# Optimization experiments

Hardware: AMD Instinct MI355X
Metric: run time of the kernel (lower is better)

Reference implementation:

```python
import jax, jax.numpy as jnp
import numpy as np

B, NQ, NKV = 2, 2048, 2048
DIM, CTX_DIM = 1024, 1024
HEADS, DIM_HEAD = 16, 64
INNER = HEADS * DIM_HEAD  # 1024
SCALE = DIM_HEAD ** -0.5


def setup_inputs() -> dict:
    key = jax.random.key(0)
    ks = jax.random.split(key, 6)
    x = jax.random.normal(ks[0], (B, NQ, DIM), dtype=jnp.float32)
    context = jax.random.normal(ks[1], (B, NKV, CTX_DIM), dtype=jnp.float32)
    # nn.Linear weights stored as [out, in] in torch; we keep [in, out] for x @ W.
    Wq = jax.random.normal(ks[2], (DIM, INNER), dtype=jnp.float32) / np.sqrt(DIM)
    Wkv = jax.random.normal(ks[3], (CTX_DIM, 2 * INNER), dtype=jnp.float32) / np.sqrt(CTX_DIM)
    Wout = jax.random.normal(ks[4], (INNER, DIM), dtype=jnp.float32) / np.sqrt(INNER)
    bout = jax.random.normal(ks[5], (DIM,), dtype=jnp.float32) * 0.01
    return {"x": x, "context": context, "Wq": Wq, "Wkv": Wkv, "Wout": Wout, "bout": bout}


def reference(x, context, Wq, Wkv, Wout, bout):
    q = x @ Wq                      # [B, Nq, inner]
    kv = context @ Wkv              # [B, Nkv, 2*inner]
    k, v = jnp.split(kv, 2, axis=-1)

    def split_heads(t):             # [B, N, inner] -> [B, H, N, dh]
        return t.reshape(t.shape[0], t.shape[1], HEADS, DIM_HEAD).transpose(0, 2, 1, 3)

    q, k, v = split_heads(q), split_heads(k), split_heads(v)
    dots = jnp.einsum('bhqd,bhkd->bhqk', q, k) * SCALE  # [B, H, Nq, Nkv]
    attn = jax.nn.softmax(dots, axis=-1)
    out = jnp.einsum('bhqk,bhkd->bhqd', attn, v)        # [B, H, Nq, dh]
    out = out.transpose(0, 2, 1, 3).reshape(out.shape[0], out.shape[2], INNER)
    return out @ Wout + bout        # [B, Nq, dim]
```

## Files before the change

### kernel.cpp

```cpp
#include <hip/hip_runtime.h>
#include <hip/hip_bf16.h>
#include <stdint.h>

#define NQ 2048
#define NKV 2048
#define DIM 1024
#define INNER 1024
#define HEADS 16
#define DH 64
#define BATCH 2

typedef float f32x4 __attribute__((ext_vector_type(4)));
typedef __bf16 bf16x8 __attribute__((ext_vector_type(8)));
typedef unsigned int u32x4 __attribute__((ext_vector_type(4)));

__device__ inline ushort f2b(float f) {
    uint32_t u = __builtin_bit_cast(uint32_t, f);
    u += 0x7fff + ((u >> 16) & 1);
    return (ushort)(u >> 16);
}

__device__ inline uint pkbf16(float lo, float hi) {
    __hip_bfloat162 h = __float22bfloat162_rn(make_float2(lo, hi));
    uint r;
    __builtin_memcpy(&r, &h, 4);
    return r;
}

__device__ __forceinline__ void gload16(const void* g, void* lds) {
    __builtin_amdgcn_global_load_lds(
        (const __attribute__((address_space(1))) unsigned int*)g,
        (__attribute__((address_space(3))) unsigned int*)lds, 16, 0, 0);
}

__global__ void cvt_f32_bf16(const float* __restrict__ in, ushort* __restrict__ out, int n4) {
    int i = blockIdx.x * blockDim.x + threadIdx.x;
    int stride = gridDim.x * blockDim.x;
    for (; i < n4; i += stride) {
        float4 v = ((const float4*)in)[i];
        ushort4 o;
        o.x = f2b(v.x); o.y = f2b(v.y); o.z = f2b(v.z); o.w = f2b(v.w);
        ((ushort4*)out)[i] = o;
    }
}

__global__ void transp_cvt(const float* __restrict__ in, ushort* __restrict__ out, int R, int C) {
    __shared__ ushort tile[32][33];
    int c0 = blockIdx.x * 32, r0 = blockIdx.y * 32;
    int tx = threadIdx.x, ty = threadIdx.y;
#pragma unroll
    for (int i = 0; i < 4; i++)
        tile[ty + i * 8][tx] = f2b(in[(size_t)(r0 + ty + i * 8) * C + c0 + tx]);
    __syncthreads();
#pragma unroll
    for (int i = 0; i < 4; i++)
        out[(size_t)(c0 + ty + i * 8) * R + r0 + tx] = tile[tx][ty + i * 8];
}

__global__ __launch_bounds__(256) void vtransp(const ushort* __restrict__ vb, ushort* __restrict__ vtb) {
    __shared__ ushort tile[64][72];
    int kt = blockIdx.x, h = blockIdx.y, b = blockIdx.z;
    int t = threadIdx.x;
    const ushort* src = vb + ((size_t)b * NKV + kt * 64) * INNER + h * DH;
#pragma unroll
    for (int p = 0; p < 2; p++) {
        int kv = p * 32 + (t >> 3), c0 = (t & 7) * 8;
        u32x4 v = *(const u32x4*)&src[(size_t)kv * INNER + c0];
        *(u32x4*)&tile[kv][c0] = v;
    }
    __syncthreads();
    ushort* dst = vtb + (((size_t)b * HEADS + h) * DH) * NKV + kt * 64;
#pragma unroll
    for (int p = 0; p < 2; p++) {
        int d = p * 32 + (t >> 3), k0 = (t & 7) * 8;
        ushort tmp[8];
#pragma unroll
        for (int j = 0; j < 8; j++) tmp[j] = tile[k0 + j][d];
        *(u32x4*)&dst[(size_t)d * NKV + k0] = *(u32x4*)tmp;
    }
}

template <int MODE, int BN>
__global__ __launch_bounds__(256) void gemm_bt(const ushort* __restrict__ A, const ushort* __restrict__ Bt,
                                               void* __restrict__ C0, void* __restrict__ C1,
                                               const float* __restrict__ bias, float oscale,
                                               int M, int N, int K) {
    constexpr int NI = BN / 32;
    __shared__ ushort As[2][4096];
    __shared__ ushort Bs[2][BN * 32];
    int m0 = blockIdx.y * 128, n0 = blockIdx.x * BN;
    int t = threadIdx.x, l = t & 63, w = t >> 6;
    int wr = w >> 1, wc = w & 1;
    int lg = l >> 4, lc = l & 15;
    f32x4 acc[4][NI] = {};

    auto stage = [&](int buf, int k0) {
#pragma unroll
        for (int i = 0; i < 2; i++) {
            int s = w + i * 4;
            gload16(A + (size_t)(m0 + (s & 1) * 64 + l) * K + k0 + (s >> 1) * 8, &As[buf][s * 512]);
        }
        if (BN == 128) {
#pragma unroll
            for (int i = 0; i < 2; i++) {
                int s = w + i * 4;
                gload16(Bt + (size_t)(n0 + (s & 1) * 64 + l) * K + k0 + (s >> 1) * 8, &Bs[buf][s * 512]);
            }
        } else {
            gload16(Bt + (size_t)(n0 + l) * K + k0 + w * 8, &Bs[buf][w * 512]);
        }
    };

    stage(0, 0);
    for (int k0 = 0, tt = 0; k0 < K; k0 += 32, ++tt) {
        __syncthreads();
        int cur = tt & 1;
        if (k0 + 32 < K) stage(cur ^ 1, k0 + 32);
        bf16x8 af[4], bf[NI];
#pragma unroll
        for (int mi = 0; mi < 4; mi++)
            af[mi] = *(const bf16x8*)&As[cur][(lg * 128 + wr * 64 + mi * 16 + lc) * 8];
#pragma unroll
        for (int ni = 0; ni < NI; ni++)
            bf[ni] = *(const bf16x8*)&Bs[cur][(lg * BN + wc * (BN / 2) + ni * 16 + lc) * 8];
        __builtin_amdgcn_s_setprio(1);
#pragma unroll
        for (int mi = 0; mi < 4; mi++)
#pragma unroll
            for (int ni = 0; ni < NI; ni++)
                acc[mi][ni] = __builtin_amdgcn_mfma_f32_16x16x32_bf16(af[mi], bf[ni], acc[mi][ni], 0, 0, 0);
        __builtin_amdgcn_s_setprio(0);
    }
#pragma unroll
    for (int mi = 0; mi < 4; mi++)
#pragma unroll
        for (int ni = 0; ni < NI; ni++)
#pragma unroll
            for (int r = 0; r < 4; r++) {
                int m = m0 + wr * 64 + mi * 16 + lg * 4 + r;
                int n = n0 + wc * (BN / 2) + ni * 16 + lc;
                float v = acc[mi][ni][r];
                if (MODE == 0) {
                    ((ushort*)C0)[(size_t)m * N + n] = f2b(v * oscale);
                } else if (MODE == 1) {
                    if (n < 1024) ((ushort*)C0)[(size_t)m * 1024 + n] = f2b(v);
                    else          ((ushort*)C1)[(size_t)m * 1024 + (n - 1024)] = f2b(v);
                } else {
                    ((float*)C0)[(size_t)m * N + n] = v + bias[n];
                }
            }
}

__global__ __launch_bounds__(256, 3) void attn3(const ushort* __restrict__ qb, const ushort* __restrict__ kb,
                                                const ushort* __restrict__ vtb, ushort* __restrict__ ob) {
    __shared__ ushort Qs[8 * 128 * 8];
    __shared__ ushort Ks[2][4096];
    __shared__ ushort Vs[2][4096];
    uint* Psw = (uint*)Qs;
    int flat = blockIdx.x;
    int swz = (flat & 7) * 64 + (flat >> 3);
    int qt = swz & 15, h = (swz >> 4) & 15, b = swz >> 8;
    int t = threadIdx.x, l = t & 63, w = t >> 6;
    int lg = l >> 4, lc = l & 15;
    int xsw = (lc << 1) & 0x1C;
    const ushort* Qg = qb + (size_t)b * NQ * INNER + h * DH;
    const ushort* Kg = kb + (size_t)b * NKV * INNER + h * DH;
    const ushort* Vg = vtb + (((size_t)b * HEADS + h) * DH) * NKV;
    int q0 = qt * 128;

#pragma unroll
    for (int i = 0; i < 4; i++) {
        int s = w * 4 + i;
        gload16(Qg + (size_t)(q0 + (s & 1) * 64 + l) * INNER + (s >> 1) * 8, &Qs[s * 512]);
    }
    auto stageKV = [&](int buf, int kv0) {
#pragma unroll
        for (int i = 0; i < 2; i++) {
            int s = w + i * 4;
            gload16(Kg + (size_t)(kv0 + l) * INNER + s * 8, &Ks[buf][s * 512]);
            gload16(Vg + (size_t)l * NKV + kv0 + s * 8, &Vs[buf][s * 512]);
        }
    };
    stageKV(0, 0);
    __syncthreads();

    bf16x8 qf[2][2];
#pragma unroll
    for (int mi = 0; mi < 2; mi++)
#pragma unroll
        for (int kc = 0; kc < 2; kc++)
            qf[mi][kc] = *(const bf16x8*)&Qs[((kc * 4 + lg) * 128 + w * 32 + mi * 16 + lc) * 8];
    __syncthreads();

    uint* Ps = Psw + w * 1024;
    f32x4 o[2][4] = {};
    float m_[2] = {-1e30f, -1e30f}, s_[2] = {0.f, 0.f};

    for (int tt = 0; tt < NKV / 64; ++tt) {
        int cur = tt & 1;
        if (tt + 1 < NKV / 64) stageKV(cur ^ 1, (tt + 1) * 64);
        f32x4 st[2][4] = {};
        __builtin_amdgcn_s_setprio(1);
#pragma unroll
        for (int kc = 0; kc < 2; kc++)
#pragma unroll
            for (int nb = 0; nb < 4; nb++) {
                bf16x8 kf = *(const bf16x8*)&Ks[cur][((kc * 4 + lg) * 64 + nb * 16 + lc) * 8];
                st[0][nb] = __builtin_amdgcn_mfma_f32_16x16x32_bf16(kf, qf[0][kc], st[0][nb], 0, 0, 0);
                st[1][nb] = __builtin_amdgcn_mfma_f32_16x16x32_bf16(kf, qf[1][kc], st[1][nb], 0, 0, 0);
            }
        __builtin_amdgcn_s_setprio(0);
#pragma unroll
        for (int mi = 0; mi < 2; mi++) {
            float mx = st[mi][0][0];
#pragma unroll
            for (int nb = 0; nb < 4; nb++)
#pragma unroll
                for (int r = 0; r < 4; r++) mx = fmaxf(mx, st[mi][nb][r]);
            mx = fmaxf(mx, __shfl_xor(mx, 16));
            mx = fmaxf(mx, __shfl_xor(mx, 32));
            float mn = fmaxf(m_[mi], mx);
            float fac = __builtin_amdgcn_exp2f(m_[mi] - mn);
            m_[mi] = mn;
            s_[mi] *= fac;
#pragma unroll
            for (int nb = 0; nb < 4; nb++) o[mi][nb] *= fac;
            float rs = 0.f;
#pragma unroll
            for (int nb = 0; nb < 4; nb++) {
                float p0 = __builtin_amdgcn_exp2f(st[mi][nb][0] - mn);
                float p1 = __builtin_amdgcn_exp2f(st[mi][nb][1] - mn);
                float p2 = __builtin_amdgcn_exp2f(st[mi][nb][2] - mn);
                float p3 = __builtin_amdgcn_exp2f(st[mi][nb][3] - mn);
                rs += (p0 + p1) + (p2 + p3);
                uint2 pw;
                pw.x = pkbf16(p0, p1);
                pw.y = pkbf16(p2, p3);
                *(uint2*)&Ps[(mi * 16 + lc) * 32 + ((nb * 8 + lg * 2) ^ xsw)] = pw;
            }
            rs += __shfl_xor(rs, 16);
            rs += __shfl_xor(rs, 32);
            s_[mi] += rs;
        }
        asm volatile("" ::: "memory");
        bf16x8 pf[2][2], vf[4][2];
#pragma unroll
        for (int mi = 0; mi < 2; mi++)
#pragma unroll
            for (int kc = 0; kc < 2; kc++)
                pf[mi][kc] = *(const bf16x8*)&Ps[(mi * 16 + lc) * 32 + ((kc * 16 + lg * 4) ^ xsw)];
#pragma unroll
        for (int nb = 0; nb < 4; nb++)
#pragma unroll
            for (int kc = 0; kc < 2; kc++)
                vf[nb][kc] = *(const bf16x8*)&Vs[cur][((kc * 4 + lg) * 64 + nb * 16 + lc) * 8];
        __builtin_amdgcn_s_setprio(1);
#pragma unroll
        for (int nb = 0; nb < 4; nb++)
#pragma unroll
            for (int kc = 0; kc < 2; kc++) {
                o[0][nb] = __builtin_amdgcn_mfma_f32_16x16x32_bf16(vf[nb][kc], pf[0][kc], o[0][nb], 0, 0, 0);
                o[1][nb] = __builtin_amdgcn_mfma_f32_16x16x32_bf16(vf[nb][kc], pf[1][kc], o[1][nb], 0, 0, 0);
            }
        __builtin_amdgcn_s_setprio(0);
        __syncthreads();
    }
    ushort* Og = ob + (size_t)b * NQ * INNER + h * DH;
#pragma unroll
    for (int mi = 0; mi < 2; mi++) {
        float inv = 1.f / s_[mi];
        int q = q0 + w * 32 + mi * 16 + lc;
#pragma unroll
        for (int nb = 0; nb < 4; nb++) {
            uint2 pw;
            pw.x = pkbf16(o[mi][nb][0] * inv, o[mi][nb][1] * inv);
            pw.y = pkbf16(o[mi][nb][2] * inv, o[mi][nb][3] * inv);
            *(uint2*)&Og[(size_t)q * INNER + nb * 16 + lg * 4] = pw;
        }
    }
}

extern "C" void kernel_launch(void* const* d_in, const int* in_sizes, int n_in,
                              void* d_out, int out_size, void* d_ws, size_t ws_size,
                              hipStream_t stream) {
    const float* x    = (const float*)d_in[0];
    const float* ctx  = (const float*)d_in[1];
    const float* Wq   = (const float*)d_in[2];
    const float* Wkv  = (const float*)d_in[3];
    const float* Wout = (const float*)d_in[4];
    const float* bout = (const float*)d_in[5];
    float* out = (float*)d_out;

    if (ws_size < (size_t)(56u << 20)) return;
    char* ws = (char*)d_ws;
    ushort* xb    = (ushort*)(ws);
    ushort* vtb   = (ushort*)(ws);
    ushort* cb    = (ushort*)(ws + (8u << 20));
    ushort* ob    = (ushort*)(ws + (8u << 20));
    ushort* qb    = (ushort*)(ws + (16u << 20));
    ushort* kb    = (ushort*)(ws + (24u << 20));
    ushort* vb    = (ushort*)(ws + (32u << 20));
    ushort* Wqt   = (ushort*)(ws + (48u << 20));
    ushort* Wkvt  = (ushort*)(ws + (50u << 20));
    ushort* Woutt = (ushort*)(ws + (54u << 20));

    cvt_f32_bf16<<<2048, 256, 0, stream>>>(x, xb, (BATCH * NQ * DIM) / 4);
    cvt_f32_bf16<<<2048, 256, 0, stream>>>(ctx, cb, (BATCH * NKV * DIM) / 4);
    transp_cvt<<<dim3(1024 / 32, 1024 / 32), dim3(32, 8), 0, stream>>>(Wq, Wqt, 1024, 1024);
    transp_cvt<<<dim3(2048 / 32, 1024 / 32), dim3(32, 8), 0, stream>>>(Wkv, Wkvt, 1024, 2048);
    transp_cvt<<<dim3(1024 / 32, 1024 / 32), dim3(32, 8), 0, stream>>>(Wout, Woutt, 1024, 1024);

    gemm_bt<0, 64><<<dim3(16, 32), 256, 0, stream>>>(xb, Wqt, qb, nullptr, nullptr, 0.125f * 1.44269504f, 4096, 1024, 1024);
    gemm_bt<1, 128><<<dim3(16, 32), 256, 0, stream>>>(cb, Wkvt, kb, vb, nullptr, 1.f, 4096, 2048, 1024);
    vtransp<<<dim3(32, 16, 2), 256, 0, stream>>>(vb, vtb);
    attn3<<<512, 256, 0, stream>>>(qb, kb, vtb, ob);
    gemm_bt<2, 64><<<dim3(16, 32), 256, 0, stream>>>(ob, Woutt, out, nullptr, bout, 1.f, 4096, 1024, 1024);
}
```

Measured before the change: 190.8 us.

## Merge prep kernels, pipeline GEMM waits, and halve attention block size

Folds the two input conversions into one launch and the three weight transposes into one 3D launch, cutting launch overhead. The GEMM mainloop replaces the leading __syncthreads with an explicit vmcnt wait that keeps the next stage's loads in flight, plus a trailing barrier. Attention moves from 256-thread blocks covering 128 queries to 128-thread blocks covering 64 queries with twice as many blocks, for more parallelism and smaller LDS per block. The added waves re-read K/V more often, and the hand-written waitcnt counts must match the number of loads issued per stage.

New measurement: 197.3 us. 1.03x slower.

```diff
diff --git a/kernel.cpp b/kernel.cpp
--- a/kernel.cpp
+++ b/kernel.cpp
@@ -33,28 +33,41 @@
         (__attribute__((address_space(3))) unsigned int*)lds, 16, 0, 0);
 }
 
-__global__ void cvt_f32_bf16(const float* __restrict__ in, ushort* __restrict__ out, int n4) {
+__global__ void cvt2(const float* __restrict__ a, ushort* __restrict__ oa,
+                     const float* __restrict__ b, ushort* __restrict__ ob, int n4) {
     int i = blockIdx.x * blockDim.x + threadIdx.x;
     int stride = gridDim.x * blockDim.x;
-    for (; i < n4; i += stride) {
-        float4 v = ((const float4*)in)[i];
+    for (; i < 2 * n4; i += stride) {
+        float4 v;
+        if (i < n4) v = ((const float4*)a)[i];
+        else        v = ((const float4*)b)[i - n4];
         ushort4 o;
         o.x = f2b(v.x); o.y = f2b(v.y); o.z = f2b(v.z); o.w = f2b(v.w);
-        ((ushort4*)out)[i] = o;
-    }
-}
-
-__global__ void transp_cvt(const float* __restrict__ in, ushort* __restrict__ out, int R, int C) {
+        if (i < n4) ((ushort4*)oa)[i] = o;
+        else        ((ushort4*)ob)[i - n4] = o;
+    }
+}
+
+__global__ void transp4(const float* __restrict__ Wq, const float* __restrict__ Wkv,
+                        const float* __restrict__ Wout,
+                        ushort* __restrict__ Wqt, ushort* __restrict__ Wkvt,
+                        ushort* __restrict__ Woutt) {
     __shared__ ushort tile[32][33];
+    int z = blockIdx.z;
+    const float* src; ushort* dst; int C;
+    if (z == 0)      { src = Wq;          dst = Wqt;                C = 1024; }
+    else if (z == 1) { src = Wkv;         dst = Wkvt;               C = 2048; }
+    else if (z == 2) { src = Wkv + 1024;  dst = Wkvt + 1024 * 1024; C = 2048; }
+    else             { src = Wout;        dst = Woutt;              C = 1024; }
     int c0 = blockIdx.x * 32, r0 = blockIdx.y * 32;
     int tx = threadIdx.x, ty = threadIdx.y;
 #pragma unroll
     for (int i = 0; i < 4; i++)
-        tile[ty + i * 8][tx] = f2b(in[(size_t)(r0 + ty + i * 8) * C + c0 + tx]);
+        tile[ty + i * 8][tx] = f2b(src[(size_t)(r0 + ty + i * 8) * C + c0 + tx]);
     __syncthreads();
 #pragma unroll
     for (int i = 0; i < 4; i++)
-        out[(size_t)(c0 + ty + i * 8) * R + r0 + tx] = tile[tx][ty + i * 8];
+        dst[(size_t)(c0 + ty + i * 8) * 1024 + r0 + tx] = tile[tx][ty + i * 8];
 }
 
 __global__ __launch_bounds__(256) void vtransp(const ushort* __restrict__ vb, ushort* __restrict__ vtb) {
@@ -86,6 +99,7 @@
                                                const float* __restrict__ bias, float oscale,
                                                int M, int N, int K) {
     constexpr int NI = BN / 32;
+    constexpr int NL = (BN == 128) ? 4 : 3;
     __shared__ ushort As[2][4096];
     __shared__ ushort Bs[2][BN * 32];
     int m0 = blockIdx.y * 128, n0 = blockIdx.x * BN;
@@ -113,9 +127,15 @@
 
     stage(0, 0);
     for (int k0 = 0, tt = 0; k0 < K; k0 += 32, ++tt) {
-        __syncthreads();
         int cur = tt & 1;
-        if (k0 + 32 < K) stage(cur ^ 1, k0 + 32);
+        if (k0 + 32 < K) {
+            stage(cur ^ 1, k0 + 32);
+            asm volatile("s_waitcnt vmcnt(%0)" :: "n"(NL) : "memory");
+        } else {
+            asm volatile("s_waitcnt vmcnt(0)" ::: "memory");
+        }
+        __builtin_amdgcn_s_barrier();
+        asm volatile("" ::: "memory");
         bf16x8 af[4], bf[NI];
 #pragma unroll
         for (int mi = 0; mi < 4; mi++)
@@ -130,6 +150,9 @@
             for (int ni = 0; ni < NI; ni++)
                 acc[mi][ni] = __builtin_amdgcn_mfma_f32_16x16x32_bf16(af[mi], bf[ni], acc[mi][ni], 0, 0, 0);
         __builtin_amdgcn_s_setprio(0);
+        asm volatile("s_waitcnt lgkmcnt(0)" ::: "memory");
+        __builtin_amdgcn_s_barrier();
+        asm volatile("" ::: "memory");
     }
 #pragma unroll
     for (int mi = 0; mi < 4; mi++)
@@ -151,32 +174,31 @@
             }
 }
 
-__global__ __launch_bounds__(256, 3) void attn3(const ushort* __restrict__ qb, const ushort* __restrict__ kb,
+__global__ __launch_bounds__(128, 2) void attn3(const ushort* __restrict__ qb, const ushort* __restrict__ kb,
                                                 const ushort* __restrict__ vtb, ushort* __restrict__ ob) {
-    __shared__ ushort Qs[8 * 128 * 8];
+    __shared__ ushort Qs[8 * 64 * 8];
     __shared__ ushort Ks[2][4096];
     __shared__ ushort Vs[2][4096];
-    uint* Psw = (uint*)Qs;
     int flat = blockIdx.x;
-    int swz = (flat & 7) * 64 + (flat >> 3);
-    int qt = swz & 15, h = (swz >> 4) & 15, b = swz >> 8;
+    int swz = (flat & 7) * 128 + (flat >> 3);
+    int qt = swz & 31, h = (swz >> 5) & 15, b = swz >> 9;
     int t = threadIdx.x, l = t & 63, w = t >> 6;
     int lg = l >> 4, lc = l & 15;
     int xsw = (lc << 1) & 0x1C;
     const ushort* Qg = qb + (size_t)b * NQ * INNER + h * DH;
     const ushort* Kg = kb + (size_t)b * NKV * INNER + h * DH;
     const ushort* Vg = vtb + (((size_t)b * HEADS + h) * DH) * NKV;
-    int q0 = qt * 128;
+    int q0 = qt * 64;
 
 #pragma unroll
     for (int i = 0; i < 4; i++) {
         int s = w * 4 + i;
-        gload16(Qg + (size_t)(q0 + (s & 1) * 64 + l) * INNER + (s >> 1) * 8, &Qs[s * 512]);
+        gload16(Qg + (size_t)(q0 + l) * INNER + s * 8, &Qs[s * 512]);
     }
     auto stageKV = [&](int buf, int kv0) {
 #pragma unroll
-        for (int i = 0; i < 2; i++) {
-            int s = w + i * 4;
+        for (int i = 0; i < 4; i++) {
+            int s = w * 4 + i;
             gload16(Kg + (size_t)(kv0 + l) * INNER + s * 8, &Ks[buf][s * 512]);
             gload16(Vg + (size_t)l * NKV + kv0 + s * 8, &Vs[buf][s * 512]);
         }
@@ -189,10 +211,10 @@
     for (int mi = 0; mi < 2; mi++)
 #pragma unroll
         for (int kc = 0; kc < 2; kc++)
-            qf[mi][kc] = *(const bf16x8*)&Qs[((kc * 4 + lg) * 128 + w * 32 + mi * 16 + lc) * 8];
+            qf[mi][kc] = *(const bf16x8*)&Qs[((kc * 4 + lg) * 64 + w * 32 + mi * 16 + lc) * 8];
     __syncthreads();
 
-    uint* Ps = Psw + w * 1024;
+    uint* Ps = (uint*)Qs + w * 1024;
     f32x4 o[2][4] = {};
     float m_[2] = {-1e30f, -1e30f}, s_[2] = {0.f, 0.f};
 
@@ -304,15 +326,12 @@
     ushort* Wkvt  = (ushort*)(ws + (50u << 20));
     ushort* Woutt = (ushort*)(ws + (54u << 20));
 
-    cvt_f32_bf16<<<2048, 256, 0, stream>>>(x, xb, (BATCH * NQ * DIM) / 4);
-    cvt_f32_bf16<<<2048, 256, 0, stream>>>(ctx, cb, (BATCH * NKV * DIM) / 4);
-    transp_cvt<<<dim3(1024 / 32, 1024 / 32), dim3(32, 8), 0, stream>>>(Wq, Wqt, 1024, 1024);
-    transp_cvt<<<dim3(2048 / 32, 1024 / 32), dim3(32, 8), 0, stream>>>(Wkv, Wkvt, 1024, 2048);
-    transp_cvt<<<dim3(1024 / 32, 1024 / 32), dim3(32, 8), 0, stream>>>(Wout, Woutt, 1024, 1024);
+    cvt2<<<2048, 256, 0, stream>>>(x, xb, ctx, cb, (BATCH * NQ * DIM) / 4);
+    transp4<<<dim3(32, 32, 4), dim3(32, 8), 0, stream>>>(Wq, Wkv, Wout, Wqt, Wkvt, Woutt);
 
     gemm_bt<0, 64><<<dim3(16, 32), 256, 0, stream>>>(xb, Wqt, qb, nullptr, nullptr, 0.125f * 1.44269504f, 4096, 1024, 1024);
     gemm_bt<1, 128><<<dim3(16, 32), 256, 0, stream>>>(cb, Wkvt, kb, vb, nullptr, 1.f, 4096, 2048, 1024);
     vtransp<<<dim3(32, 16, 2), 256, 0, stream>>>(vb, vtb);
-    attn3<<<512, 256, 0, stream>>>(qb, kb, vtb, ob);
+    attn3<<<1024, 128, 0, stream>>>(qb, kb, vtb, ob);
     gemm_bt<2, 64><<<dim3(16, 32), 256, 0, stream>>>(ob, Woutt, out, nullptr, bout, 1.f, 4096, 1024, 1024);
 }
```
